# Kernel tuning notes

Hardware: AMD Instinct MI355X
Metric: run time of the kernel (lower is better)

The kernel has to match this reference:

```python
import jax, jax.numpy as jnp
import numpy as np

CORE_DIM = 128
MEMORY_SLOTS = 64
B, S = 4, 4096


def setup_inputs() -> dict:
    key = jax.random.key(0)
    k1, k2, k3, k4, k5 = jax.random.split(key, 5)
    x = jax.random.normal(k1, (B, S, CORE_DIM), dtype=jnp.float32)
    memory_keys = jax.random.normal(k2, (MEMORY_SLOTS, CORE_DIM), dtype=jnp.float32)
    memory_ops = jax.random.normal(k3, (MEMORY_SLOTS, CORE_DIM, CORE_DIM), dtype=jnp.float32)
    # nn.Linear(core_dim, core_dim): weight [out, in], bias [out]
    bound = 1.0 / np.sqrt(CORE_DIM)
    Wq = jax.random.uniform(k4, (CORE_DIM, CORE_DIM), minval=-bound, maxval=bound, dtype=jnp.float32)
    bq = jax.random.uniform(k5, (CORE_DIM,), minval=-bound, maxval=bound, dtype=jnp.float32)
    return {"input_tensor": x, "memory_keys": memory_keys, "memory_ops": memory_ops, "Wq": Wq, "bq": bq}


def reference(input_tensor, memory_keys, memory_ops, Wq, bq):
    dim = input_tensor.shape[-1]
    # query projection: x @ Wq^T + bq
    queries = jnp.einsum('bsd,ed->bse', input_tensor, Wq) + bq
    # soft attention over memory slots
    attn_logits = jnp.einsum('bsd,md->bsm', queries, memory_keys)
    attn_weights = jax.nn.softmax(attn_logits / jnp.sqrt(jnp.float32(dim)), axis=-1)
    # fused: (sum_m attn[bsm] * ops[m]) @ x[bs]  == sum_m attn[bsm] * (ops[m] @ x[bs])
    processed = jnp.einsum('bsm,mde,bse->bsd', attn_weights, memory_ops, input_tensor)
    return processed
```

## Files before the change

kernel.cpp:

```cpp
#include <hip/hip_runtime.h>

typedef __bf16 bf16x8 __attribute__((ext_vector_type(8)));
typedef float f32x4 __attribute__((ext_vector_type(4)));
typedef unsigned int uint4v __attribute__((ext_vector_type(4)));
typedef unsigned short ushort_t;
typedef unsigned int uint_t;

#define RS 0.08838834764831845f

__device__ __forceinline__ ushort_t f2bf(float f) {
    uint_t u = __float_as_uint(f);
    u += 0x7FFFu + ((u >> 16) & 1u);
    return (ushort_t)(u >> 16);
}
__device__ __forceinline__ uint_t pack2(float a, float b) {
    return (uint_t)f2bf(a) | ((uint_t)f2bf(b) << 16);
}
union U4B8 { uint4v u; bf16x8 b; };
__device__ __forceinline__ bf16x8 as_bf(uint4v u) { U4B8 x; x.u = u; return x.b; }

__device__ __forceinline__ int xfrag(int f, int lane) {
    return f * 1072 + ((lane >> 4) * 272) + ((lane & 15) * 16);
}

__global__ __launch_bounds__(256) void prep_kernel(
    const float* __restrict__ ops, const float* __restrict__ keys,
    const float* __restrict__ Wq, const float* __restrict__ bq,
    uint4v* __restrict__ ops_sw, ushort_t* __restrict__ kp_sw,
    float* __restrict__ cb)
{
    const int tid = threadIdx.x;
    const int b = blockIdx.x;
    if (b >= 64) {
        int g = (b - 64) * 256 + tid;
        int L = g & 63, dt = (g >> 6) & 7, ks = (g >> 9) & 3, m = g >> 11;
        int d = dt * 16 + (L & 15);
        int e0 = ks * 32 + ((L >> 4) << 3);
        const float4* s = (const float4*)(ops + (((size_t)(m * 128 + d)) << 7) + e0);
        float4 v0 = s[0], v1 = s[1];
        uint4v o = { pack2(v0.x, v0.y), pack2(v0.z, v0.w),
                     pack2(v1.x, v1.y), pack2(v1.z, v1.w) };
        ops_sw[g] = o;
    } else {
        __shared__ float red[256];
        const int m = b;
        const int d = tid & 127, eh = tid >> 7;
        const float* kr = keys + m * 128 + eh * 64;
        const float* wc = Wq + (size_t)(eh * 64) * 128 + d;
        float acc = 0.f;
        #pragma unroll 8
        for (int e = 0; e < 64; ++e)
            acc = fmaf(kr[e], wc[(size_t)e * 128], acc);
        red[tid] = acc;
        __syncthreads();
        if (tid < 128) {
            float v = red[tid] + red[tid + 128];
            int ki = d >> 5, qq = (d >> 3) & 3, j = d & 7;
            kp_sw[((((ki * 4 + (m >> 4)) * 64) + (qq * 16 + (m & 15))) << 3) | j] = f2bf(v);
        } else if (tid >= 192) {
            int lane = tid - 192;
            float p = keys[m * 128 + lane] * bq[lane]
                    + keys[m * 128 + 64 + lane] * bq[64 + lane];
            #pragma unroll
            for (int off = 1; off < 64; off <<= 1) p += __shfl_xor(p, off);
            if (lane == 0) cb[m] = p;
        }
    }
}

__global__ __launch_bounds__(256, 2) void main_kernel(
    const float* __restrict__ x, const float* __restrict__ cb,
    const ushort_t* __restrict__ kp_sw, const uint4v* __restrict__ ops_sw,
    float* __restrict__ out)
{
    __shared__ __align__(16) unsigned char xs[17152];
    __shared__ float attn_f[64 * 68];

    const int tid = threadIdx.x;
    const int lane = tid & 63;
    const int w = tid >> 6;
    const int q = lane >> 4;
    const int l15 = lane & 15;
    const int tb = blockIdx.x >> 1;
    const int dh = blockIdx.x & 1;
    const int t0 = tb * 64;
    const int dtw = dh * 4 + w;

    {
        const float4* x4 = (const float4*)(x + (size_t)t0 * 128);
        #pragma unroll
        for (int it = 0; it < 4; ++it) {
            int i = it * 256 + tid;
            int t = i >> 4, kc = i & 15;
            float4 a = x4[t * 32 + kc * 2];
            float4 b2 = x4[t * 32 + kc * 2 + 1];
            uint4v o = { pack2(a.x, a.y), pack2(a.z, a.w),
                         pack2(b2.x, b2.y), pack2(b2.z, b2.w) };
            *(uint4v*)(xs + ((t >> 4) * 4 + (kc >> 2)) * 1072
                          + (kc & 3) * 272 + (t & 15) * 16) = o;
        }
    }
    __syncthreads();

    {
        f32x4 L0 = {0,0,0,0}, L1 = {0,0,0,0}, L2 = {0,0,0,0}, L3 = {0,0,0,0};
        const uint4v* kpf = (const uint4v*)kp_sw;
        #pragma unroll
        for (int ki = 0; ki < 4; ++ki) {
            bf16x8 a = *(const bf16x8*)(xs + xfrag(w * 4 + ki, lane));
            L0 = __builtin_amdgcn_mfma_f32_16x16x32_bf16(a, as_bf(kpf[(ki*4+0)*64 + lane]), L0, 0,0,0);
            L1 = __builtin_amdgcn_mfma_f32_16x16x32_bf16(a, as_bf(kpf[(ki*4+1)*64 + lane]), L1, 0,0,0);
            L2 = __builtin_amdgcn_mfma_f32_16x16x32_bf16(a, as_bf(kpf[(ki*4+2)*64 + lane]), L2, 0,0,0);
            L3 = __builtin_amdgcn_mfma_f32_16x16x32_bf16(a, as_bf(kpf[(ki*4+3)*64 + lane]), L3, 0,0,0);
        }
        float c0 = cb[l15], c1 = cb[16 + l15], c2 = cb[32 + l15], c3 = cb[48 + l15];
        #pragma unroll
        for (int r = 0; r < 4; ++r) {
            float v0 = (L0[r] + c0) * RS;
            float v1 = (L1[r] + c1) * RS;
            float v2 = (L2[r] + c2) * RS;
            float v3 = (L3[r] + c3) * RS;
            float mx = fmaxf(fmaxf(v0, v1), fmaxf(v2, v3));
            #pragma unroll
            for (int off = 1; off < 16; off <<= 1) mx = fmaxf(mx, __shfl_xor(mx, off));
            float e0 = __expf(v0 - mx), e1 = __expf(v1 - mx),
                  e2 = __expf(v2 - mx), e3 = __expf(v3 - mx);
            float sm = e0 + e1 + e2 + e3;
            #pragma unroll
            for (int off = 1; off < 16; off <<= 1) sm += __shfl_xor(sm, off);
            float inv = 1.0f / sm;
            int t = w * 16 + q * 4 + r;
            attn_f[(     l15) * 68 + t] = e0 * inv;
            attn_f[(16 + l15) * 68 + t] = e1 * inv;
            attn_f[(32 + l15) * 68 + t] = e2 * inv;
            attn_f[(48 + l15) * 68 + t] = e3 * inv;
        }
    }

    bf16x8 A[4][4];
    #pragma unroll
    for (int tf = 0; tf < 4; ++tf)
        #pragma unroll
        for (int ki = 0; ki < 4; ++ki)
            A[tf][ki] = *(const bf16x8*)(xs + xfrag(tf * 4 + ki, lane));

    __syncthreads();

    const uint4v* ob = ops_sw + (size_t)dtw * 64 + lane;
    f32x4 C[4] = {};
    uint4v B0[4], B1[4];
    #pragma unroll
    for (int ki = 0; ki < 4; ++ki) B0[ki] = ob[ki * 512];

    for (int ml = 0; ml < 64; ml += 2) {
        {
            const uint4v* pn = ob + (size_t)(ml + 1) * 2048;
            #pragma unroll
            for (int ki = 0; ki < 4; ++ki) B1[ki] = pn[ki * 512];
            f32x4 S[4] = {};
            #pragma unroll
            for (int ki = 0; ki < 4; ++ki) {
                bf16x8 bfrag = as_bf(B0[ki]);
                #pragma unroll
                for (int tf = 0; tf < 4; ++tf)
                    S[tf] = __builtin_amdgcn_mfma_f32_16x16x32_bf16(A[tf][ki], bfrag, S[tf], 0,0,0);
            }
            #pragma unroll
            for (int tf = 0; tf < 4; ++tf) {
                f32x4 af = *(const f32x4*)&attn_f[ml * 68 + tf * 16 + q * 4];
                #pragma unroll
                for (int r = 0; r < 4; ++r)
                    C[tf][r] = fmaf(af[r], S[tf][r], C[tf][r]);
            }
        }
        {
            const int mn = (ml + 2 < 64) ? ml + 2 : 63;
            const uint4v* pn = ob + (size_t)mn * 2048;
            #pragma unroll
            for (int ki = 0; ki < 4; ++ki) B0[ki] = pn[ki * 512];
            f32x4 S[4] = {};
            #pragma unroll
            for (int ki = 0; ki < 4; ++ki) {
                bf16x8 bfrag = as_bf(B1[ki]);
                #pragma unroll
                for (int tf = 0; tf < 4; ++tf)
                    S[tf] = __builtin_amdgcn_mfma_f32_16x16x32_bf16(A[tf][ki], bfrag, S[tf], 0,0,0);
            }
            #pragma unroll
            for (int tf = 0; tf < 4; ++tf) {
                f32x4 af = *(const f32x4*)&attn_f[(ml + 1) * 68 + tf * 16 + q * 4];
                #pragma unroll
                for (int r = 0; r < 4; ++r)
                    C[tf][r] = fmaf(af[r], S[tf][r], C[tf][r]);
            }
        }
    }

    float* op = out + (size_t)t0 * 128 + dh * 64 + w * 16 + l15;
    #pragma unroll
    for (int tf = 0; tf < 4; ++tf)
        #pragma unroll
        for (int r = 0; r < 4; ++r)
            op[(size_t)(tf * 16 + q * 4 + r) * 128] = C[tf][r];
}

extern "C" void kernel_launch(void* const* d_in, const int* in_sizes, int n_in,
                              void* d_out, int out_size, void* d_ws, size_t ws_size,
                              hipStream_t stream)
{
    const float* x    = (const float*)d_in[0];
    const float* keys = (const float*)d_in[1];
    const float* ops  = (const float*)d_in[2];
    const float* Wq   = (const float*)d_in[3];
    const float* bq   = (const float*)d_in[4];
    float* out = (float*)d_out;

    char* ws = (char*)d_ws;
    uint4v*   ops_sw = (uint4v*)ws;
    ushort_t* kp_sw  = (ushort_t*)(ws + 2097152);
    float*    cb     = (float*)(ws + 2097152 + 16384);

    prep_kernel<<<576, 256, 0, stream>>>(ops, keys, Wq, bq, ops_sw, kp_sw, cb);
    main_kernel<<<512, 256, 0, stream>>>(x, cb, kp_sw, ops_sw, out);
}
```

Measured before the change: 120.0 us.

## Use 512-thread blocks covering 128 tokens and 32 output columns per block

```diff
diff --git a/kernel.cpp b/kernel.cpp
--- a/kernel.cpp
+++ b/kernel.cpp
@@ -7,6 +7,7 @@
 typedef unsigned int uint_t;
 
 #define RS 0.08838834764831845f
+#define APF 133
 
 __device__ __forceinline__ ushort_t f2bf(float f) {
     uint_t u = __float_as_uint(f);
@@ -68,29 +69,31 @@
     }
 }
 
-__global__ __launch_bounds__(256, 2) void main_kernel(
+__global__ __launch_bounds__(512, 4) void main_kernel(
     const float* __restrict__ x, const float* __restrict__ cb,
     const ushort_t* __restrict__ kp_sw, const uint4v* __restrict__ ops_sw,
     float* __restrict__ out)
 {
-    __shared__ __align__(16) unsigned char xs[17152];
-    __shared__ float attn_f[64 * 68];
+    __shared__ __align__(16) unsigned char xs[34304];
+    __shared__ float attn_f[64 * APF];
 
     const int tid = threadIdx.x;
     const int lane = tid & 63;
     const int w = tid >> 6;
     const int q = lane >> 4;
     const int l15 = lane & 15;
-    const int tb = blockIdx.x >> 1;
-    const int dh = blockIdx.x & 1;
-    const int t0 = tb * 64;
-    const int dtw = dh * 4 + w;
+    const int tb = blockIdx.x >> 2;
+    const int dq4 = blockIdx.x & 3;
+    const int t0 = tb * 128;
+    const int tq = w & 3;
+    const int dt2 = w >> 2;
+    const int dtile = dq4 * 2 + dt2;
 
     {
         const float4* x4 = (const float4*)(x + (size_t)t0 * 128);
         #pragma unroll
         for (int it = 0; it < 4; ++it) {
-            int i = it * 256 + tid;
+            int i = it * 512 + tid;
             int t = i >> 4, kc = i & 15;
             float4 a = x4[t * 32 + kc * 2];
             float4 b2 = x4[t * 32 + kc * 2 + 1];
@@ -130,24 +133,25 @@
             for (int off = 1; off < 16; off <<= 1) sm += __shfl_xor(sm, off);
             float inv = 1.0f / sm;
             int t = w * 16 + q * 4 + r;
-            attn_f[(     l15) * 68 + t] = e0 * inv;
-            attn_f[(16 + l15) * 68 + t] = e1 * inv;
-            attn_f[(32 + l15) * 68 + t] = e2 * inv;
-            attn_f[(48 + l15) * 68 + t] = e3 * inv;
-        }
-    }
-
-    bf16x8 A[4][4];
+            attn_f[(     l15) * APF + t] = e0 * inv;
+            attn_f[(16 + l15) * APF + t] = e1 * inv;
+            attn_f[(32 + l15) * APF + t] = e2 * inv;
+            attn_f[(48 + l15) * APF + t] = e3 * inv;
+        }
+    }
+
+    bf16x8 A[2][4];
     #pragma unroll
-    for (int tf = 0; tf < 4; ++tf)
+    for (int tg = 0; tg < 2; ++tg)
         #pragma unroll
         for (int ki = 0; ki < 4; ++ki)
-            A[tf][ki] = *(const bf16x8*)(xs + xfrag(tf * 4 + ki, lane));
+            A[tg][ki] = *(const bf16x8*)(xs + xfrag((tq * 2 + tg) * 4 + ki, lane));
 
     __syncthreads();
 
-    const uint4v* ob = ops_sw + (size_t)dtw * 64 + lane;
-    f32x4 C[4] = {};
+    const uint4v* ob = ops_sw + (size_t)dtile * 64 + lane;
+    const float* af_base = attn_f + tq * 32 + q * 4;
+    f32x4 C[2] = {};
     uint4v B0[4], B1[4];
     #pragma unroll
     for (int ki = 0; ki < 4; ++ki) B0[ki] = ob[ki * 512];
@@ -157,20 +161,19 @@
             const uint4v* pn = ob + (size_t)(ml + 1) * 2048;
             #pragma unroll
             for (int ki = 0; ki < 4; ++ki) B1[ki] = pn[ki * 512];
-            f32x4 S[4] = {};
+            f32x4 S[2] = {};
             #pragma unroll
             for (int ki = 0; ki < 4; ++ki) {
                 bf16x8 bfrag = as_bf(B0[ki]);
-                #pragma unroll
-                for (int tf = 0; tf < 4; ++tf)
-                    S[tf] = __builtin_amdgcn_mfma_f32_16x16x32_bf16(A[tf][ki], bfrag, S[tf], 0,0,0);
-            }
-            #pragma unroll
-            for (int tf = 0; tf < 4; ++tf) {
-                f32x4 af = *(const f32x4*)&attn_f[ml * 68 + tf * 16 + q * 4];
+                S[0] = __builtin_amdgcn_mfma_f32_16x16x32_bf16(A[0][ki], bfrag, S[0], 0,0,0);
+                S[1] = __builtin_amdgcn_mfma_f32_16x16x32_bf16(A[1][ki], bfrag, S[1], 0,0,0);
+            }
+            #pragma unroll
+            for (int tg = 0; tg < 2; ++tg) {
+                f32x4 af = *(const f32x4*)(af_base + ml * APF + tg * 16);
                 #pragma unroll
                 for (int r = 0; r < 4; ++r)
-                    C[tf][r] = fmaf(af[r], S[tf][r], C[tf][r]);
+                    C[tg][r] = fmaf(af[r], S[tg][r], C[tg][r]);
             }
         }
         {
@@ -178,30 +181,29 @@
             const uint4v* pn = ob + (size_t)mn * 2048;
             #pragma unroll
             for (int ki = 0; ki < 4; ++ki) B0[ki] = pn[ki * 512];
-            f32x4 S[4] = {};
+            f32x4 S[2] = {};
             #pragma unroll
             for (int ki = 0; ki < 4; ++ki) {
                 bf16x8 bfrag = as_bf(B1[ki]);
-                #pragma unroll
-                for (int tf = 0; tf < 4; ++tf)
-                    S[tf] = __builtin_amdgcn_mfma_f32_16x16x32_bf16(A[tf][ki], bfrag, S[tf], 0,0,0);
-            }
-            #pragma unroll
-            for (int tf = 0; tf < 4; ++tf) {
-                f32x4 af = *(const f32x4*)&attn_f[(ml + 1) * 68 + tf * 16 + q * 4];
+                S[0] = __builtin_amdgcn_mfma_f32_16x16x32_bf16(A[0][ki], bfrag, S[0], 0,0,0);
+                S[1] = __builtin_amdgcn_mfma_f32_16x16x32_bf16(A[1][ki], bfrag, S[1], 0,0,0);
+            }
+            #pragma unroll
+            for (int tg = 0; tg < 2; ++tg) {
+                f32x4 af = *(const f32x4*)(af_base + (ml + 1) * APF + tg * 16);
                 #pragma unroll
                 for (int r = 0; r < 4; ++r)
-                    C[tf][r] = fmaf(af[r], S[tf][r], C[tf][r]);
-            }
-        }
-    }
-
-    float* op = out + (size_t)t0 * 128 + dh * 64 + w * 16 + l15;
+                    C[tg][r] = fmaf(af[r], S[tg][r], C[tg][r]);
+            }
+        }
+    }
+
+    float* op = out + (size_t)(t0 + tq * 32) * 128 + dtile * 16 + l15;
     #pragma unroll
-    for (int tf = 0; tf < 4; ++tf)
+    for (int tg = 0; tg < 2; ++tg)
         #pragma unroll
         for (int r = 0; r < 4; ++r)
-            op[(size_t)(tf * 16 + q * 4 + r) * 128] = C[tf][r];
+            op[(size_t)(tg * 16 + q * 4 + r) * 128] = C[tg][r];
 }
 
 extern "C" void kernel_launch(void* const* d_in, const int* in_sizes, int n_in,
@@ -221,5 +223,5 @@
     float*    cb     = (float*)(ws + 2097152 + 16384);
 
     prep_kernel<<<576, 256, 0, stream>>>(ops, keys, Wq, bq, ops_sw, kp_sw, cb);
-    main_kernel<<<512, 256, 0, stream>>>(x, cb, kp_sw, ops_sw, out);
-}
+    main_kernel<<<512, 512, 0, stream>>>(x, cb, kp_sw, ops_sw, out);
+}
```

New measurement: 124.9 us. 1.04x slower.
